# Kernel tuning notes

Measured on AMD Instinct MI355X. Metric: run time of the kernel, lower is better.

## Reference

```python
import jax, jax.numpy as jnp
import numpy as np

N = 100000
E = 3200000
D_IN = 256
D_OUT = 256


def setup_inputs() -> dict:
    key = jax.random.key(0)
    kx, ke1, ke2, kw = jax.random.split(key, 4)
    X = jax.random.normal(kx, (N, D_IN), dtype=jnp.float32)
    src = jax.random.randint(ke1, (E,), 0, N, dtype=jnp.int64)
    dst = jax.random.randint(ke2, (E,), 0, N, dtype=jnp.int64)
    # avoid pre-existing self-loops so fill_diag(adj, 1) == appending unit self-loops
    dst = jnp.where(src == dst, (dst + 1) % N, dst)
    edge_index = jnp.stack([src, dst], axis=0)
    W = jax.random.normal(kw, (D_IN, D_OUT), dtype=jnp.float32) * (1.0 / np.sqrt(D_IN))
    return {"X": X, "edge_index": edge_index, "W": W}


def reference(X, edge_index, W):
    # A_tilde = A (unit edge values) with unit self-loops on the diagonal
    loop = jnp.arange(N, dtype=edge_index.dtype)
    row = jnp.concatenate([edge_index[0], loop])
    col = jnp.concatenate([edge_index[1], loop])
    vals = jnp.ones(row.shape[0], dtype=X.dtype)

    # D_tilde = rowsum(A_tilde); D^{-1/2} with inf -> 0
    deg = jax.ops.segment_sum(vals, row, num_segments=N)
    dinv = jnp.where(deg > 0, deg ** -0.5, 0.0)

    # Faithful to source: both mul() calls use unsqueeze(0) (column scaling),
    # so A_hat[i,j] = A_tilde[i,j] * dinv[j]^2
    norm = vals * dinv[col] * dinv[col]

    # SpMM: out_i = sum_{e: row_e = i} norm_e * X[col_e]
    agg = jax.ops.segment_sum(norm[:, None] * X[col], row, num_segments=N)
    return agg @ W
```

## Files before the change

### kernel.cpp

```cpp
#include <hip/hip_runtime.h>

#define NN 100000
#define NE 3200000
#define DD 256
#define NCHUNK 98

static __device__ __forceinline__ unsigned short f2bf(float f) {
    unsigned u = __float_as_uint(f);
    return (unsigned short)((u + 0x7fffu + ((u >> 16) & 1u)) >> 16);
}
static __device__ __forceinline__ float bflo(unsigned v) { return __uint_as_float(v << 16); }
static __device__ __forceinline__ float bfhi(unsigned v) { return __uint_as_float(v & 0xffff0000u); }

__global__ void k_init_deg(int* __restrict__ deg) {
    int i = blockIdx.x * 256 + threadIdx.x;
    if (i < NN) deg[i] = 1;
}

__global__ void k_count(const int* __restrict__ src, int* __restrict__ deg) {
    int stride = gridDim.x * blockDim.x;
    for (int e = blockIdx.x * blockDim.x + threadIdx.x; e < NE; e += stride)
        atomicAdd(&deg[src[e]], 1);
}

__global__ void k_chunksum(const int* __restrict__ deg, int* __restrict__ csum) {
    __shared__ int s[256];
    int b = blockIdx.x, t = threadIdx.x;
    int base = b * 1024 + t * 4;
    int sum = 0;
#pragma unroll
    for (int j = 0; j < 4; ++j) {
        int i = base + j;
        if (i < NN) sum += deg[i] - 1;
    }
    s[t] = sum;
    __syncthreads();
    for (int d = 128; d > 0; d >>= 1) {
        if (t < d) s[t] += s[t + d];
        __syncthreads();
    }
    if (t == 0) csum[b] = s[0];
}

__global__ void k_scanchunks(int* __restrict__ csum) {
    if (blockIdx.x == 0 && threadIdx.x == 0) {
        int run = 0;
        for (int c = 0; c < NCHUNK; ++c) {
            int v = csum[c];
            csum[c] = run;
            run += v;
        }
    }
}

__global__ void k_scanwithin(const int* __restrict__ deg, const int* __restrict__ csum,
                             int* __restrict__ offs, int* __restrict__ woff,
                             float* __restrict__ dinv) {
    __shared__ int s[256];
    int b = blockIdx.x, t = threadIdx.x;
    int base = b * 1024 + t * 4;
    int c[4];
#pragma unroll
    for (int j = 0; j < 4; ++j) {
        int i = base + j;
        c[j] = (i < NN) ? deg[i] - 1 : 0;
    }
    int tsum = c[0] + c[1] + c[2] + c[3];
    s[t] = tsum;
    __syncthreads();
    for (int d = 1; d < 256; d <<= 1) {
        int v = (t >= d) ? s[t - d] : 0;
        __syncthreads();
        s[t] += v;
        __syncthreads();
    }
    int run = s[t] - tsum + csum[b];
#pragma unroll
    for (int j = 0; j < 4; ++j) {
        int i = base + j;
        if (i < NN) {
            offs[i] = run;
            woff[i] = run;
            dinv[i] = 1.0f / (float)deg[i];
            run += c[j];
        }
    }
}

__global__ void k_scatter(const int* __restrict__ src, const int* __restrict__ dst,
                          const float* __restrict__ dinv,
                          int* __restrict__ woff, int2* __restrict__ ejw) {
    int stride = gridDim.x * blockDim.x;
    for (int e = blockIdx.x * blockDim.x + threadIdx.x; e < NE; e += stride) {
        int s = src[e];
        int d = dst[e];
        float w = dinv[d];
        int pos = atomicAdd(&woff[s], 1);
        ejw[pos] = make_int2(d, __float_as_int(w));
    }
}

__global__ void k_wt(const float* __restrict__ W, unsigned short* __restrict__ Wt) {
    int idx = blockIdx.x * 256 + threadIdx.x;
    int n = idx >> 8, k = idx & 255;
    Wt[n * 256 + k] = f2bf(W[k * 256 + n]);
}

__global__ __launch_bounds__(256) void k_gemm(const float* __restrict__ X,
                                              const unsigned short* __restrict__ Wt,
                                              unsigned short* __restrict__ Y) {
    using bf16x8 = __attribute__((ext_vector_type(8))) short;
    using f32x4 = __attribute__((ext_vector_type(4))) float;
    __shared__ unsigned short As[32 * 40];
    __shared__ unsigned short Bs[256 * 40];

    int tid = threadIdx.x;
    int lane = tid & 63, w = tid >> 6;
    int row0 = blockIdx.x * 32;

    f32x4 acc[2][4];
#pragma unroll
    for (int m = 0; m < 2; ++m)
#pragma unroll
        for (int nt = 0; nt < 4; ++nt) acc[m][nt] = (f32x4){0.f, 0.f, 0.f, 0.f};

    int ar = tid >> 3;
    int ak = (tid & 7) * 4;
    int mrow = lane & 15, quad = lane >> 4;

    for (int k0 = 0; k0 < 256; k0 += 32) {
        float4 xv = *(const float4*)(X + (size_t)(row0 + ar) * 256 + k0 + ak);
        ushort4 xb;
        xb.x = f2bf(xv.x); xb.y = f2bf(xv.y); xb.z = f2bf(xv.z); xb.w = f2bf(xv.w);
        *(ushort4*)&As[ar * 40 + ak] = xb;
#pragma unroll
        for (int it = 0; it < 4; ++it) {
            int g = it * 256 + tid;
            int n = g >> 2, kq = g & 3;
            uint4 bv = *(const uint4*)(Wt + (size_t)n * 256 + k0 + kq * 8);
            *(uint4*)&Bs[n * 40 + kq * 8] = bv;
        }
        __syncthreads();

        bf16x8 af[2], bfr[4];
#pragma unroll
        for (int m = 0; m < 2; ++m)
            af[m] = *(const bf16x8*)&As[(m * 16 + mrow) * 40 + quad * 8];
#pragma unroll
        for (int nt = 0; nt < 4; ++nt)
            bfr[nt] = *(const bf16x8*)&Bs[(w * 64 + nt * 16 + mrow) * 40 + quad * 8];
#pragma unroll
        for (int m = 0; m < 2; ++m)
#pragma unroll
            for (int nt = 0; nt < 4; ++nt)
                acc[m][nt] = __builtin_amdgcn_mfma_f32_16x16x32_bf16(af[m], bfr[nt], acc[m][nt], 0, 0, 0);
        __syncthreads();
    }

#pragma unroll
    for (int m = 0; m < 2; ++m)
#pragma unroll
        for (int nt = 0; nt < 4; ++nt)
#pragma unroll
            for (int r = 0; r < 4; ++r) {
                int row = row0 + m * 16 + quad * 4 + r;
                int col = w * 64 + nt * 16 + mrow;
                Y[(size_t)row * 256 + col] = f2bf(acc[m][nt][r]);
            }
}

__global__ __launch_bounds__(256) void k_spmm(const uint2* __restrict__ Yp,
                                              const int2* __restrict__ ejw,
                                              const int* __restrict__ offs,
                                              const int* __restrict__ deg,
                                              const float* __restrict__ dinv,
                                              float* __restrict__ out) {
    int w = threadIdx.x >> 6;
    int lane = threadIdx.x & 63;
    int i = blockIdx.x * 4 + w;

    float wi = dinv[i];
    uint2 v = Yp[(size_t)i * 64 + lane];
    float a0 = bflo(v.x) * wi, a1 = bfhi(v.x) * wi;
    float a2 = bflo(v.y) * wi, a3 = bfhi(v.y) * wi;

    int off = offs[i];
    int cnt = deg[i] - 1;
    const int2* e = ejw + off;

    for (int k = 0; k < cnt; k += 4) {
        int2 p[4];
        float wj[4];
#pragma unroll
        for (int u = 0; u < 4; ++u) {
            int idx = k + u;
            int cl = idx < cnt ? idx : cnt - 1;
            p[u] = e[cl];
            wj[u] = (idx < cnt) ? __int_as_float(p[u].y) : 0.f;
        }
        uint2 r[4];
#pragma unroll
        for (int u = 0; u < 4; ++u) r[u] = Yp[(size_t)p[u].x * 64 + lane];
#pragma unroll
        for (int u = 0; u < 4; ++u) {
            a0 = fmaf(bflo(r[u].x), wj[u], a0);
            a1 = fmaf(bfhi(r[u].x), wj[u], a1);
            a2 = fmaf(bflo(r[u].y), wj[u], a2);
            a3 = fmaf(bfhi(r[u].y), wj[u], a3);
        }
    }

    *(float4*)(out + (size_t)i * 256 + lane * 4) = make_float4(a0, a1, a2, a3);
}

extern "C" void kernel_launch(void* const* d_in, const int* in_sizes, int n_in,
                              void* d_out, int out_size, void* d_ws, size_t ws_size,
                              hipStream_t stream) {
    const float* X = (const float*)d_in[0];
    const int* ei = (const int*)d_in[1];
    const float* W = (const float*)d_in[2];
    const int* src = ei;
    const int* dst = ei + NE;
    float* out = (float*)d_out;

    char* p = (char*)d_ws;
    auto alloc = [&](size_t bytes) {
        void* r = (void*)p;
        p += (bytes + 511) & ~(size_t)511;
        return r;
    };
    int* deg = (int*)alloc((size_t)NN * 4);
    int* offs = (int*)alloc((size_t)NN * 4);
    int* woff = (int*)alloc((size_t)NN * 4);
    int* csum = (int*)alloc((size_t)NCHUNK * 4);
    float* dinv = (float*)alloc((size_t)NN * 4);
    int2* ejw = (int2*)alloc(((size_t)NE + 8) * 8);
    unsigned short* Wt = (unsigned short*)alloc((size_t)DD * DD * 2);
    unsigned short* Y = (unsigned short*)alloc((size_t)NN * DD * 2);

    k_init_deg<<<(NN + 255) / 256, 256, 0, stream>>>(deg);
    k_count<<<2048, 256, 0, stream>>>(src, deg);
    k_chunksum<<<NCHUNK, 256, 0, stream>>>(deg, csum);
    k_scanchunks<<<1, 64, 0, stream>>>(csum);
    k_scanwithin<<<NCHUNK, 256, 0, stream>>>(deg, csum, offs, woff, dinv);
    k_scatter<<<2048, 256, 0, stream>>>(src, dst, dinv, woff, ejw);
    k_wt<<<DD * DD / 256, 256, 0, stream>>>(W, Wt);
    k_gemm<<<NN / 32, 256, 0, stream>>>(X, Wt, Y);
    k_spmm<<<NN / 4, 256, 0, stream>>>((const uint2*)Y, ejw, offs, deg, dinv, out);
}
```

Before: 734.9 us.

## Prescale GEMM output by dinv, store index-only adjacency, persistent register-resident-W GEMM

The GEMM becomes a persistent kernel that keeps the bf16 W fragments in registers, double-buffers whole 32-row X tiles in LDS, and multiplies each output row by dinv before writing Z. Because of that prescale, the scatter only writes destination indices (4 bytes instead of 8), and the SpMM becomes a plain sum over Z rows with an 8-way unrolled gather. Smaller changes ride along: the count and scatter kernels use one thread per edge instead of grid-stride loops, and the chunk scan becomes a parallel scan. The aim is to cut edge-list traffic, drop per-edge multiplies and avoid reloading W per tile, at the cost of heavy register pressure in the GEMM.

```diff
diff --git a/kernel.cpp b/kernel.cpp
--- a/kernel.cpp
+++ b/kernel.cpp
@@ -4,6 +4,8 @@
 #define NE 3200000
 #define DD 256
 #define NCHUNK 98
+#define NTILES 3125
+#define GGRID 512
 
 static __device__ __forceinline__ unsigned short f2bf(float f) {
     unsigned u = __float_as_uint(f);
@@ -18,9 +20,8 @@
 }
 
 __global__ void k_count(const int* __restrict__ src, int* __restrict__ deg) {
-    int stride = gridDim.x * blockDim.x;
-    for (int e = blockIdx.x * blockDim.x + threadIdx.x; e < NE; e += stride)
-        atomicAdd(&deg[src[e]], 1);
+    int e = blockIdx.x * 256 + threadIdx.x;
+    atomicAdd(&deg[src[e]], 1);
 }
 
 __global__ void k_chunksum(const int* __restrict__ deg, int* __restrict__ csum) {
@@ -43,14 +44,18 @@
 }
 
 __global__ void k_scanchunks(int* __restrict__ csum) {
-    if (blockIdx.x == 0 && threadIdx.x == 0) {
-        int run = 0;
-        for (int c = 0; c < NCHUNK; ++c) {
-            int v = csum[c];
-            csum[c] = run;
-            run += v;
-        }
-    }
+    __shared__ int s[128];
+    int t = threadIdx.x;
+    int v = (t < NCHUNK) ? csum[t] : 0;
+    s[t] = v;
+    __syncthreads();
+    for (int d = 1; d < 128; d <<= 1) {
+        int u = (t >= d) ? s[t - d] : 0;
+        __syncthreads();
+        s[t] += u;
+        __syncthreads();
+    }
+    if (t < NCHUNK) csum[t] = s[t] - v;
 }
 
 __global__ void k_scanwithin(const int* __restrict__ deg, const int* __restrict__ csum,
@@ -88,16 +93,11 @@
 }
 
 __global__ void k_scatter(const int* __restrict__ src, const int* __restrict__ dst,
-                          const float* __restrict__ dinv,
-                          int* __restrict__ woff, int2* __restrict__ ejw) {
-    int stride = gridDim.x * blockDim.x;
-    for (int e = blockIdx.x * blockDim.x + threadIdx.x; e < NE; e += stride) {
-        int s = src[e];
-        int d = dst[e];
-        float w = dinv[d];
-        int pos = atomicAdd(&woff[s], 1);
-        ejw[pos] = make_int2(d, __float_as_int(w));
-    }
+                          int* __restrict__ woff, int* __restrict__ adj) {
+    int e = blockIdx.x * 256 + threadIdx.x;
+    int s = src[e];
+    int pos = atomicAdd(&woff[s], 1);
+    adj[pos] = dst[e];
 }
 
 __global__ void k_wt(const float* __restrict__ W, unsigned short* __restrict__ Wt) {
@@ -106,107 +106,148 @@
     Wt[n * 256 + k] = f2bf(W[k * 256 + n]);
 }
 
-__global__ __launch_bounds__(256) void k_gemm(const float* __restrict__ X,
-                                              const unsigned short* __restrict__ Wt,
-                                              unsigned short* __restrict__ Y) {
+__global__ __launch_bounds__(256, 2) void k_gemm(const float* __restrict__ X,
+                                                 const unsigned short* __restrict__ Wt,
+                                                 const float* __restrict__ dinv,
+                                                 unsigned short* __restrict__ Z) {
     using bf16x8 = __attribute__((ext_vector_type(8))) short;
     using f32x4 = __attribute__((ext_vector_type(4))) float;
-    __shared__ unsigned short As[32 * 40];
-    __shared__ unsigned short Bs[256 * 40];
+    __shared__ unsigned short As[2][32 * 264];
 
     int tid = threadIdx.x;
     int lane = tid & 63, w = tid >> 6;
-    int row0 = blockIdx.x * 32;
-
-    f32x4 acc[2][4];
-#pragma unroll
-    for (int m = 0; m < 2; ++m)
-#pragma unroll
-        for (int nt = 0; nt < 4; ++nt) acc[m][nt] = (f32x4){0.f, 0.f, 0.f, 0.f};
-
-    int ar = tid >> 3;
-    int ak = (tid & 7) * 4;
     int mrow = lane & 15, quad = lane >> 4;
 
-    for (int k0 = 0; k0 < 256; k0 += 32) {
-        float4 xv = *(const float4*)(X + (size_t)(row0 + ar) * 256 + k0 + ak);
-        ushort4 xb;
-        xb.x = f2bf(xv.x); xb.y = f2bf(xv.y); xb.z = f2bf(xv.z); xb.w = f2bf(xv.w);
-        *(ushort4*)&As[ar * 40 + ak] = xb;
-#pragma unroll
-        for (int it = 0; it < 4; ++it) {
-            int g = it * 256 + tid;
-            int n = g >> 2, kq = g & 3;
-            uint4 bv = *(const uint4*)(Wt + (size_t)n * 256 + k0 + kq * 8);
-            *(uint4*)&Bs[n * 40 + kq * 8] = bv;
-        }
-        __syncthreads();
-
-        bf16x8 af[2], bfr[4];
+    bf16x8 Bf[4][8];
+#pragma unroll
+    for (int nt = 0; nt < 4; ++nt)
+#pragma unroll
+        for (int k0 = 0; k0 < 8; ++k0)
+            Bf[nt][k0] = *(const bf16x8*)(Wt + (size_t)(w * 64 + nt * 16 + mrow) * 256 + k0 * 32 + quad * 8);
+
+    const float4* X4 = (const float4*)X;
+    float4 sreg[8];
+
+    auto load_tile = [&](int t) {
+        int row0 = t * 32;
+#pragma unroll
+        for (int jj = 0; jj < 8; ++jj) {
+            int g = jj * 256 + tid;
+            int r = g >> 6, k4 = g & 63;
+            sreg[jj] = X4[(size_t)(row0 + r) * 64 + k4];
+        }
+    };
+    auto store_tile = [&](int buf) {
+#pragma unroll
+        for (int jj = 0; jj < 8; ++jj) {
+            int g = jj * 256 + tid;
+            int r = g >> 6, k4 = g & 63;
+            ushort4 h;
+            h.x = f2bf(sreg[jj].x);
+            h.y = f2bf(sreg[jj].y);
+            h.z = f2bf(sreg[jj].z);
+            h.w = f2bf(sreg[jj].w);
+            *(ushort4*)&As[buf][r * 264 + k4 * 4] = h;
+        }
+    };
+
+    int t = blockIdx.x;
+    load_tile(t);
+    store_tile(0);
+    __syncthreads();
+    int buf = 0;
+
+    for (;;) {
+        int tn = t + GGRID;
+        bool hn = tn < NTILES;
+        if (hn) load_tile(tn);
+
+        f32x4 acc[2][4];
 #pragma unroll
         for (int m = 0; m < 2; ++m)
-            af[m] = *(const bf16x8*)&As[(m * 16 + mrow) * 40 + quad * 8];
-#pragma unroll
-        for (int nt = 0; nt < 4; ++nt)
-            bfr[nt] = *(const bf16x8*)&Bs[(w * 64 + nt * 16 + mrow) * 40 + quad * 8];
-#pragma unroll
-        for (int m = 0; m < 2; ++m)
-#pragma unroll
-            for (int nt = 0; nt < 4; ++nt)
-                acc[m][nt] = __builtin_amdgcn_mfma_f32_16x16x32_bf16(af[m], bfr[nt], acc[m][nt], 0, 0, 0);
-        __syncthreads();
-    }
-
-#pragma unroll
-    for (int m = 0; m < 2; ++m)
-#pragma unroll
-        for (int nt = 0; nt < 4; ++nt)
-#pragma unroll
-            for (int r = 0; r < 4; ++r) {
-                int row = row0 + m * 16 + quad * 4 + r;
+#pragma unroll
+            for (int nt = 0; nt < 4; ++nt) acc[m][nt] = (f32x4){0.f, 0.f, 0.f, 0.f};
+
+#pragma unroll
+        for (int k0 = 0; k0 < 8; ++k0) {
+            bf16x8 af0 = *(const bf16x8*)&As[buf][(mrow) * 264 + k0 * 32 + quad * 8];
+            bf16x8 af1 = *(const bf16x8*)&As[buf][(16 + mrow) * 264 + k0 * 32 + quad * 8];
+#pragma unroll
+            for (int nt = 0; nt < 4; ++nt) {
+                acc[0][nt] = __builtin_amdgcn_mfma_f32_16x16x32_bf16(af0, Bf[nt][k0], acc[0][nt], 0, 0, 0);
+                acc[1][nt] = __builtin_amdgcn_mfma_f32_16x16x32_bf16(af1, Bf[nt][k0], acc[1][nt], 0, 0, 0);
+            }
+        }
+
+        int row0 = t * 32;
+#pragma unroll
+        for (int m = 0; m < 2; ++m) {
+            int rbase = row0 + m * 16 + quad * 4;
+            float4 dv = *(const float4*)&dinv[rbase];
+            float dva[4] = {dv.x, dv.y, dv.z, dv.w};
+#pragma unroll
+            for (int nt = 0; nt < 4; ++nt) {
                 int col = w * 64 + nt * 16 + mrow;
-                Y[(size_t)row * 256 + col] = f2bf(acc[m][nt][r]);
+#pragma unroll
+                for (int r = 0; r < 4; ++r)
+                    Z[(size_t)(rbase + r) * 256 + col] = f2bf(acc[m][nt][r] * dva[r]);
             }
-}
-
-__global__ __launch_bounds__(256) void k_spmm(const uint2* __restrict__ Yp,
-                                              const int2* __restrict__ ejw,
+        }
+
+        if (!hn) break;
+        store_tile(buf ^ 1);
+        __syncthreads();
+        buf ^= 1;
+        t = tn;
+    }
+}
+
+__global__ __launch_bounds__(256) void k_spmm(const uint2* __restrict__ Zp,
+                                              const int* __restrict__ adj,
                                               const int* __restrict__ offs,
                                               const int* __restrict__ deg,
-                                              const float* __restrict__ dinv,
                                               float* __restrict__ out) {
     int w = threadIdx.x >> 6;
     int lane = threadIdx.x & 63;
     int i = blockIdx.x * 4 + w;
 
-    float wi = dinv[i];
-    uint2 v = Yp[(size_t)i * 64 + lane];
-    float a0 = bflo(v.x) * wi, a1 = bfhi(v.x) * wi;
-    float a2 = bflo(v.y) * wi, a3 = bfhi(v.y) * wi;
+    uint2 v = Zp[(size_t)i * 64 + lane];
+    float a0 = bflo(v.x), a1 = bfhi(v.x);
+    float a2 = bflo(v.y), a3 = bfhi(v.y);
 
     int off = offs[i];
     int cnt = deg[i] - 1;
-    const int2* e = ejw + off;
-
-    for (int k = 0; k < cnt; k += 4) {
-        int2 p[4];
-        float wj[4];
-#pragma unroll
-        for (int u = 0; u < 4; ++u) {
-            int idx = k + u;
+    const int* e = adj + off;
+    int kmain = cnt & ~7;
+
+    for (int k = 0; k < kmain; k += 8) {
+        int j[8];
+#pragma unroll
+        for (int u = 0; u < 8; ++u) j[u] = e[k + u];
+        uint2 r[8];
+#pragma unroll
+        for (int u = 0; u < 8; ++u) r[u] = Zp[(size_t)j[u] * 64 + lane];
+#pragma unroll
+        for (int u = 0; u < 8; ++u) {
+            a0 += bflo(r[u].x);
+            a1 += bfhi(r[u].x);
+            a2 += bflo(r[u].y);
+            a3 += bfhi(r[u].y);
+        }
+    }
+    if (kmain < cnt) {
+#pragma unroll
+        for (int u = 0; u < 8; ++u) {
+            int idx = kmain + u;
             int cl = idx < cnt ? idx : cnt - 1;
-            p[u] = e[cl];
-            wj[u] = (idx < cnt) ? __int_as_float(p[u].y) : 0.f;
-        }
-        uint2 r[4];
-#pragma unroll
-        for (int u = 0; u < 4; ++u) r[u] = Yp[(size_t)p[u].x * 64 + lane];
-#pragma unroll
-        for (int u = 0; u < 4; ++u) {
-            a0 = fmaf(bflo(r[u].x), wj[u], a0);
-            a1 = fmaf(bfhi(r[u].x), wj[u], a1);
-            a2 = fmaf(bflo(r[u].y), wj[u], a2);
-            a3 = fmaf(bfhi(r[u].y), wj[u], a3);
+            int j = e[cl];
+            uint2 r = Zp[(size_t)j * 64 + lane];
+            if (idx < cnt) {
+                a0 += bflo(r.x);
+                a1 += bfhi(r.x);
+                a2 += bflo(r.y);
+                a3 += bfhi(r.y);
+            }
         }
     }
 
@@ -234,17 +275,17 @@
     int* woff = (int*)alloc((size_t)NN * 4);
     int* csum = (int*)alloc((size_t)NCHUNK * 4);
     float* dinv = (float*)alloc((size_t)NN * 4);
-    int2* ejw = (int2*)alloc(((size_t)NE + 8) * 8);
+    int* adj = (int*)alloc(((size_t)NE + 16) * 4);
     unsigned short* Wt = (unsigned short*)alloc((size_t)DD * DD * 2);
-    unsigned short* Y = (unsigned short*)alloc((size_t)NN * DD * 2);
+    unsigned short* Z = (unsigned short*)alloc((size_t)NN * DD * 2);
 
     k_init_deg<<<(NN + 255) / 256, 256, 0, stream>>>(deg);
-    k_count<<<2048, 256, 0, stream>>>(src, deg);
+    k_count<<<NE / 256, 256, 0, stream>>>(src, deg);
     k_chunksum<<<NCHUNK, 256, 0, stream>>>(deg, csum);
-    k_scanchunks<<<1, 64, 0, stream>>>(csum);
+    k_scanchunks<<<1, 128, 0, stream>>>(csum);
     k_scanwithin<<<NCHUNK, 256, 0, stream>>>(deg, csum, offs, woff, dinv);
-    k_scatter<<<2048, 256, 0, stream>>>(src, dst, dinv, woff, ejw);
     k_wt<<<DD * DD / 256, 256, 0, stream>>>(W, Wt);
-    k_gemm<<<NN / 32, 256, 0, stream>>>(X, Wt, Y);
-    k_spmm<<<NN / 4, 256, 0, stream>>>((const uint2*)Y, ejw, offs, deg, dinv, out);
-}
+    k_gemm<<<GGRID, 256, 0, stream>>>(X, Wt, dinv, Z);
+    k_scatter<<<NE / 256, 256, 0, stream>>>(src, dst, woff, adj);
+    k_spmm<<<NN / 4, 256, 0, stream>>>((const uint2*)Z, adj, offs, deg, out);
+}
```

New measurement: 819.2 us. +11.5%, slower.
